# Kernel optimization log

Hardware: AMD Instinct MI355X
Metric: run time of the kernel (lower is better)

## Reference

```python
import jax, jax.numpy as jnp
import numpy as np
from jax import lax

B, T, E, V, U = 128, 80, 100, 10000, 512


def setup_inputs() -> dict:
    key = jax.random.key(0)
    ks = jax.random.split(key, 10)
    s = 0.05
    return {
        "tokens": jax.random.randint(ks[0], (B, T), 0, V, dtype=jnp.int32),
        "emb": jax.random.normal(ks[1], (V, E), jnp.float32) * s,
        "k0": jax.random.normal(ks[2], (E, U), jnp.float32) * s,   # cell0 input kernel
        "rk0": jax.random.normal(ks[3], (U, U), jnp.float32) * s,  # cell0 recurrent kernel
        "b0": jnp.zeros((U,), jnp.float32),
        "k1": jax.random.normal(ks[4], (U, U), jnp.float32) * s,   # cell1 input kernel
        "rk1": jax.random.normal(ks[5], (U, U), jnp.float32) * s,
        "b1": jnp.zeros((U,), jnp.float32),
        "wd": jax.random.normal(ks[6], (U, 1), jnp.float32) * s,   # output Dense
        "bd": jnp.zeros((1,), jnp.float32),
    }


def reference(tokens, emb, k0, rk0, b0, k1, rk1, b1, wd, bd):
    # Embedding lookup: [B, T, E]
    x = emb[tokens]
    xs = jnp.swapaxes(x, 0, 1)  # [T, B, E] for scan over time

    # Source quirk: `state0 = state1` after each step, so from step 1 onward
    # BOTH cells recur on cell1's previous hidden state h. Carry is a single h.
    def step(h, word):
        h0 = jnp.tanh(word @ k0 + h @ rk0 + b0)  # SimpleRNNCell 0 (dropout off: training=None)
        h1 = jnp.tanh(h0 @ k1 + h @ rk1 + b1)    # SimpleRNNCell 1
        return h1, None

    h_init = jnp.zeros((B, U), x.dtype)
    h_last, _ = lax.scan(step, h_init, xs)

    logits = h_last @ wd + bd  # [B, 1]
    return jax.nn.sigmoid(logits)
```

## Files before the change

kernel.cpp:

```cpp
#include <hip/hip_runtime.h>


typedef __attribute__((ext_vector_type(8))) short short8;
typedef __attribute__((ext_vector_type(4))) float f32x4;

#define MFMA16(a,b,c) __builtin_amdgcn_mfma_f32_16x16x32_bf16(a,b,c,0,0,0)
#define LOAD_RLX(p)    __hip_atomic_load((p), __ATOMIC_RELAXED, __HIP_MEMORY_SCOPE_AGENT)
#define STORE_RLX(p,v) __hip_atomic_store((p), (v), __ATOMIC_RELAXED, __HIP_MEMORY_SCOPE_AGENT)
#define ADD_RLX(p,v)   __hip_atomic_fetch_add((p), (v), __ATOMIC_RELAXED, __HIP_MEMORY_SCOPE_AGENT)

__device__ __forceinline__ short f2bf(float v){
  unsigned u = __float_as_uint(v);
  u = (u + 0x7fffu + ((u >> 16) & 1u)) >> 16;
  return (short)u;
}
__device__ __forceinline__ float bf2f(short s){
  return __uint_as_float(((unsigned)(unsigned short)s) << 16);
}
__device__ __forceinline__ float fast_tanh(float x){
  x = fminf(15.f, fmaxf(-15.f, x));
  float e = __expf(2.f * x);
  return (e - 1.f) * __builtin_amdgcn_rcpf(e + 1.f);
}

__launch_bounds__(128, 1)
__global__ void rnn_kernel(const int* __restrict__ tokens,
                           const float* __restrict__ emb,
                           const float* __restrict__ k0,
                           const float* __restrict__ rk0,
                           const float* __restrict__ b0,
                           const float* __restrict__ k1,
                           const float* __restrict__ rk1,
                           const float* __restrict__ b1,
                           const float* __restrict__ wd,
                           const float* __restrict__ bd,
                           float* __restrict__ out,
                           char* __restrict__ ws)
{
  constexpr int T = 80, E = 100, U = 512;
  const int tid  = threadIdx.x;
  const int w    = tid >> 6;
  const int lane = tid & 63;
  const int m    = lane & 15;
  const int q    = lane >> 4;

  __shared__ __align__(16) short sW[6][16][520];
  __shared__ __align__(16) short sH[2][16][520];
  __shared__ __align__(16) short sE[2][16][136];
  __shared__ __align__(16) short sK0[2][16][136];
  __shared__ int   sTok[16][80];
  __shared__ float sB0[16], sB1[16];
  __shared__ float sRed[16][8];
  __shared__ int   sReg[2];

  int*      regCnt = (int*)(ws + 512);
  int*      flags  = (int*)(ws + 4096);
  unsigned* hPk    = (unsigned*)(ws + 40960);
  unsigned* h0Pk   = hPk + 128*U;

  int xcc;
  asm volatile("s_getreg_b32 %0, hwreg(HW_REG_XCC_ID)" : "=s"(xcc));
  if (tid == 0){
    int slot = ADD_RLX(regCnt + (xcc & 7)*16, 1);
    sReg[0] = xcc & 7;
    sReg[1] = slot;
  }
  __syncthreads();
  const int cl  = sReg[0];
  const int mem = sReg[1];
  int* const myFlag   = flags + (cl*32 + mem)*32;
  int* const pollAddr = flags + (cl*32 + (lane & 31))*32;

  const float* mats[3] = { rk0, rk1, k1 };
  for (int mi = 0; mi < 3; ++mi){
    const float* G = mats[mi];
    for (int i = tid; i < 16*U; i += 128){
      int k = i >> 4, c = i & 15;
      float v  = G[k*U + mem*16 + c];
      short hi = f2bf(v);
      short lo = f2bf(v - bf2f(hi));
      sW[2*mi+0][c][k] = hi;
      sW[2*mi+1][c][k] = lo;
    }
  }
  for (int i = tid; i < 2*16*136; i += 128){ ((short*)sE)[i] = 0; ((short*)sK0)[i] = 0; }
  __syncthreads();
  for (int i = tid; i < 16*E; i += 128){
    int e = i >> 4, c = i & 15;
    float v  = k0[e*U + mem*16 + c];
    short hi = f2bf(v);
    short lo = f2bf(v - bf2f(hi));
    sK0[0][c][e] = hi; sK0[1][c][e] = lo;
  }
  for (int i = tid; i < 16*T; i += 128){
    int r = i / T, t = i - r*T;
    sTok[r][t] = tokens[(cl*16 + r)*T + t];
  }
  if (tid < 16){ sB0[tid] = b0[mem*16 + tid]; sB1[tid] = b1[mem*16 + tid]; }
  __syncthreads();

  auto post = [&](int val){
    asm volatile("s_waitcnt vmcnt(0)" ::: "memory");
    if (lane == 0) STORE_RLX(myFlag, val);
  };
  auto pollFlags = [&](int target){
    while (__any(LOAD_RLX(pollAddr) < target)) {}
  };
  auto gather = [&](const unsigned* srcPk){
    const uint4* s = (const uint4*)(srcPk + cl*16*U);
    uint4 r[16];
    #pragma unroll
    for (int j = 0; j < 16; ++j)
      asm volatile("global_load_dwordx4 %0, %1, off sc0"
                   : "=v"(r[j]) : "v"(&s[j*128 + tid]));
    asm volatile("s_waitcnt vmcnt(0)" ::: "memory");
    #pragma unroll
    for (int j = 0; j < 16; ++j){
      int i = j*128 + tid, row = i >> 7, c = (i & 127) * 4;
      unsigned h0 = (r[j].x >> 16)     | (r[j].y & 0xffff0000u);
      unsigned h1 = (r[j].z >> 16)     | (r[j].w & 0xffff0000u);
      unsigned l0 = (r[j].x & 0xffffu) | (r[j].y << 16);
      unsigned l1 = (r[j].z & 0xffffu) | (r[j].w << 16);
      uint2 hh; hh.x = h0; hh.y = h1;
      uint2 ll; ll.x = l0; ll.y = l1;
      *(uint2*)&sH[0][row][c] = hh;
      *(uint2*)&sH[1][row][c] = ll;
    }
  };

  const f32x4 zero4 = {0.f, 0.f, 0.f, 0.f};

  for (int t = 0; t < T; ++t){
    if (w == 1){
      float ev[25];
      #pragma unroll
      for (int p = 0; p < 25; ++p){
        int i = lane + p*64;
        ev[p] = emb[sTok[i/E][t]*E + (i % E)];
      }
      #pragma unroll
      for (int p = 0; p < 25; ++p){
        int i = lane + p*64;
        int row = i / E, e = i % E;
        short hi = f2bf(ev[p]);
        short lo = f2bf(ev[p] - bf2f(hi));
        sE[0][row][e] = hi; sE[1][row][e] = lo;
      }
    } else {
      if (t > 0) pollFlags(2*t);
    }
    __syncthreads();
    if (t > 0) gather(hPk);
    __syncthreads();

    f32x4 z1a = zero4, z1b = zero4, z1c = zero4, z1d = zero4;
    if (w == 0){
      f32x4 za = zero4, zb = zero4, zc = zero4, zd = zero4;
      #pragma unroll
      for (int kk = 0; kk < 4; ++kk){
        short8 ah = *(const short8*)&sE[0][m][kk*32 + q*8];
        short8 al = *(const short8*)&sE[1][m][kk*32 + q*8];
        short8 bh = *(const short8*)&sK0[0][m][kk*32 + q*8];
        short8 bl = *(const short8*)&sK0[1][m][kk*32 + q*8];
        za = MFMA16(ah, bh, za); zb = MFMA16(al, bh, zb);
        zc = MFMA16(ah, bl, zc); zd = MFMA16(al, bl, zd);
      }
      if (t > 0){
        #pragma unroll
        for (int kk = 0; kk < 16; ++kk){
          short8 ah = *(const short8*)&sH[0][m][kk*32 + q*8];
          short8 al = *(const short8*)&sH[1][m][kk*32 + q*8];
          short8 bh = *(const short8*)&sW[0][m][kk*32 + q*8];
          short8 bl = *(const short8*)&sW[1][m][kk*32 + q*8];
          za = MFMA16(ah, bh, za); zb = MFMA16(al, bh, zb);
          zc = MFMA16(ah, bl, zc); zd = MFMA16(al, bl, zd);
        }
      }
      f32x4 z = za; z += zb; z += zc; z += zd;
      #pragma unroll
      for (int r = 0; r < 4; ++r){
        float h0v = fast_tanh(z[r] + sB0[m]);
        short hi = f2bf(h0v);
        short lo = f2bf(h0v - bf2f(hi));
        int gr = cl*16 + q*4 + r, gc = mem*16 + m;
        unsigned pk = ((unsigned)(unsigned short)hi << 16) | (unsigned short)lo;
        h0Pk[gr*U + gc] = pk;
      }
      post(2*t + 1);
    } else {
      if (t > 0){
        #pragma unroll
        for (int kk = 0; kk < 16; ++kk){
          short8 ah = *(const short8*)&sH[0][m][kk*32 + q*8];
          short8 al = *(const short8*)&sH[1][m][kk*32 + q*8];
          short8 bh = *(const short8*)&sW[2][m][kk*32 + q*8];
          short8 bl = *(const short8*)&sW[3][m][kk*32 + q*8];
          z1a = MFMA16(ah, bh, z1a); z1b = MFMA16(al, bh, z1b);
          z1c = MFMA16(ah, bl, z1c); z1d = MFMA16(al, bl, z1d);
        }
      }
    }

    if (w == 0) pollFlags(2*t + 1);
    __syncthreads();
    gather(h0Pk);
    __syncthreads();
    if (w == 1){
      f32x4 za = zero4, zb = zero4, zc = zero4, zd = zero4;
      #pragma unroll
      for (int kk = 0; kk < 16; ++kk){
        short8 ah = *(const short8*)&sH[0][m][kk*32 + q*8];
        short8 al = *(const short8*)&sH[1][m][kk*32 + q*8];
        short8 bh = *(const short8*)&sW[4][m][kk*32 + q*8];
        short8 bl = *(const short8*)&sW[5][m][kk*32 + q*8];
        za = MFMA16(ah, bh, za); zb = MFMA16(al, bh, zb);
        zc = MFMA16(ah, bl, zc); zd = MFMA16(al, bl, zd);
      }
      f32x4 z = za; z += zb; z += zc; z += zd;
      z += z1a; z += z1b; z += z1c; z += z1d;
      #pragma unroll
      for (int r = 0; r < 4; ++r){
        float h1v = fast_tanh(z[r] + sB1[m]);
        short hi = f2bf(h1v);
        short lo = f2bf(h1v - bf2f(hi));
        int gr = cl*16 + q*4 + r, gc = mem*16 + m;
        unsigned pk = ((unsigned)(unsigned short)hi << 16) | (unsigned short)lo;
        hPk[gr*U + gc] = pk;
      }
      post(2*t + 2);
    }
  }

  if (mem == 0){
    if (w == 0) pollFlags(2*T);
    __syncthreads();
    gather(hPk);
    __syncthreads();
    {
      int row = tid >> 3, seg = tid & 7;
      float acc = 0.f;
      for (int u = seg*64; u < seg*64 + 64; ++u){
        float hv = bf2f(sH[0][row][u]) + bf2f(sH[1][row][u]);
        acc += hv * wd[u];
      }
      sRed[row][seg] = acc;
    }
    __syncthreads();
    if (tid < 16){
      float s = bd[0];
      #pragma unroll
      for (int j = 0; j < 8; ++j) s += sRed[tid][j];
      out[cl*16 + tid] = 1.f / (1.f + __expf(-s));
    }
  }

  __threadfence();
}

extern "C" void kernel_launch(void* const* d_in, const int* in_sizes, int n_in,
                              void* d_out, int out_size, void* d_ws, size_t ws_size,
                              hipStream_t stream) {
  const int*   tokens = (const int*)  d_in[0];
  const float* emb    = (const float*)d_in[1];
  const float* k0     = (const float*)d_in[2];
  const float* rk0    = (const float*)d_in[3];
  const float* b0     = (const float*)d_in[4];
  const float* k1     = (const float*)d_in[5];
  const float* rk1    = (const float*)d_in[6];
  const float* b1     = (const float*)d_in[7];
  const float* wd     = (const float*)d_in[8];
  const float* bd     = (const float*)d_in[9];

  hipMemsetAsync(d_ws, 0, 40960, stream);

  hipLaunchKernelGGL(rnn_kernel, dim3(256), dim3(128), 0, stream,
                     tokens, emb, k0, rk0, b0, k1, rk1, b1, wd, bd,
                     (float*)d_out, (char*)d_ws);
}
```

Measured before the change: 625.9 us.

## Split batch rows per wavefront to remove block barriers and use independent flag chains

```diff
diff --git a/kernel.cpp b/kernel.cpp
--- a/kernel.cpp
+++ b/kernel.cpp
@@ -39,18 +39,18 @@
 {
   constexpr int T = 80, E = 100, U = 512;
   const int tid  = threadIdx.x;
-  const int w    = tid >> 6;
+  const int g    = tid >> 6;
   const int lane = tid & 63;
   const int m    = lane & 15;
   const int q    = lane >> 4;
+  const int m7   = m & 7;
 
   __shared__ __align__(16) short sW[6][16][520];
-  __shared__ __align__(16) short sH[2][16][520];
-  __shared__ __align__(16) short sE[2][16][136];
+  __shared__ __align__(16) short sH[2][2][8][520];
+  __shared__ __align__(16) short sE[2][2][8][136];
   __shared__ __align__(16) short sK0[2][16][136];
   __shared__ int   sTok[16][80];
   __shared__ float sB0[16], sB1[16];
-  __shared__ float sRed[16][8];
   __shared__ int   sReg[2];
 
   int*      regCnt = (int*)(ws + 512);
@@ -68,8 +68,8 @@
   __syncthreads();
   const int cl  = sReg[0];
   const int mem = sReg[1];
-  int* const myFlag   = flags + (cl*32 + mem)*32;
-  int* const pollAddr = flags + (cl*32 + (lane & 31))*32;
+  int* const myFlag   = flags + (cl*32 + mem)*32 + g*16;
+  int* const pollAddr = flags + (cl*32 + (lane & 31))*32 + g*16;
 
   const float* mats[3] = { rk0, rk1, k1 };
   for (int mi = 0; mi < 3; ++mi){
@@ -83,7 +83,8 @@
       sW[2*mi+1][c][k] = lo;
     }
   }
-  for (int i = tid; i < 2*16*136; i += 128){ ((short*)sE)[i] = 0; ((short*)sK0)[i] = 0; }
+  for (int i = tid; i < 2*2*8*136; i += 128) ((short*)sE)[i]  = 0;
+  for (int i = tid; i < 2*16*136;  i += 128) ((short*)sK0)[i] = 0;
   __syncthreads();
   for (int i = tid; i < 16*E; i += 128){
     int e = i >> 4, c = i & 15;
@@ -99,6 +100,11 @@
   if (tid < 16){ sB0[tid] = b0[mem*16 + tid]; sB1[tid] = b1[mem*16 + tid]; }
   __syncthreads();
 
+  short (*sHg)[8][520] = sH[g];
+  short (*sEg)[8][136] = sE[g];
+  unsigned* const hRow0  = hPk  + (cl*16 + g*8)*U;
+  unsigned* const h0Row0 = h0Pk + (cl*16 + g*8)*U;
+
   auto post = [&](int val){
     asm volatile("s_waitcnt vmcnt(0)" ::: "memory");
     if (lane == 0) STORE_RLX(myFlag, val);
@@ -106,151 +112,132 @@
   auto pollFlags = [&](int target){
     while (__any(LOAD_RLX(pollAddr) < target)) {}
   };
-  auto gather = [&](const unsigned* srcPk){
-    const uint4* s = (const uint4*)(srcPk + cl*16*U);
+  auto gather = [&](const unsigned* srcRow0){
+    const uint4* s = (const uint4*)srcRow0;
     uint4 r[16];
     #pragma unroll
     for (int j = 0; j < 16; ++j)
       asm volatile("global_load_dwordx4 %0, %1, off sc0"
-                   : "=v"(r[j]) : "v"(&s[j*128 + tid]));
+                   : "=v"(r[j]) : "v"(&s[j*64 + lane]));
     asm volatile("s_waitcnt vmcnt(0)" ::: "memory");
     #pragma unroll
     for (int j = 0; j < 16; ++j){
-      int i = j*128 + tid, row = i >> 7, c = (i & 127) * 4;
+      int i = j*64 + lane, row = i >> 7, c = (i & 127) * 4;
       unsigned h0 = (r[j].x >> 16)     | (r[j].y & 0xffff0000u);
       unsigned h1 = (r[j].z >> 16)     | (r[j].w & 0xffff0000u);
       unsigned l0 = (r[j].x & 0xffffu) | (r[j].y << 16);
       unsigned l1 = (r[j].z & 0xffffu) | (r[j].w << 16);
       uint2 hh; hh.x = h0; hh.y = h1;
       uint2 ll; ll.x = l0; ll.y = l1;
-      *(uint2*)&sH[0][row][c] = hh;
-      *(uint2*)&sH[1][row][c] = ll;
+      *(uint2*)&sHg[0][row][c] = hh;
+      *(uint2*)&sHg[1][row][c] = ll;
     }
   };
 
   const f32x4 zero4 = {0.f, 0.f, 0.f, 0.f};
 
   for (int t = 0; t < T; ++t){
-    if (w == 1){
-      float ev[25];
-      #pragma unroll
-      for (int p = 0; p < 25; ++p){
-        int i = lane + p*64;
-        ev[p] = emb[sTok[i/E][t]*E + (i % E)];
-      }
-      #pragma unroll
-      for (int p = 0; p < 25; ++p){
-        int i = lane + p*64;
-        int row = i / E, e = i % E;
+    float ev[13];
+    #pragma unroll
+    for (int p = 0; p < 13; ++p){
+      int i = lane + p*64;
+      ev[p] = (i < 800) ? emb[sTok[g*8 + i/100][t]*E + (i % 100)] : 0.f;
+    }
+    #pragma unroll
+    for (int p = 0; p < 13; ++p){
+      int i = lane + p*64;
+      if (i < 800){
+        int row = i / 100, e = i % 100;
         short hi = f2bf(ev[p]);
         short lo = f2bf(ev[p] - bf2f(hi));
-        sE[0][row][e] = hi; sE[1][row][e] = lo;
-      }
-    } else {
-      if (t > 0) pollFlags(2*t);
-    }
-    __syncthreads();
-    if (t > 0) gather(hPk);
-    __syncthreads();
-
+        sEg[0][row][e] = hi; sEg[1][row][e] = lo;
+      }
+    }
+    f32x4 za = zero4, zb = zero4, zc = zero4, zd = zero4;
+    #pragma unroll
+    for (int kk = 0; kk < 4; ++kk){
+      short8 ah = *(const short8*)&sEg[0][m7][kk*32 + q*8];
+      short8 al = *(const short8*)&sEg[1][m7][kk*32 + q*8];
+      short8 bh = *(const short8*)&sK0[0][m][kk*32 + q*8];
+      short8 bl = *(const short8*)&sK0[1][m][kk*32 + q*8];
+      za = MFMA16(ah, bh, za); zb = MFMA16(al, bh, zb);
+      zc = MFMA16(ah, bl, zc); zd = MFMA16(al, bl, zd);
+    }
     f32x4 z1a = zero4, z1b = zero4, z1c = zero4, z1d = zero4;
-    if (w == 0){
-      f32x4 za = zero4, zb = zero4, zc = zero4, zd = zero4;
-      #pragma unroll
-      for (int kk = 0; kk < 4; ++kk){
-        short8 ah = *(const short8*)&sE[0][m][kk*32 + q*8];
-        short8 al = *(const short8*)&sE[1][m][kk*32 + q*8];
-        short8 bh = *(const short8*)&sK0[0][m][kk*32 + q*8];
-        short8 bl = *(const short8*)&sK0[1][m][kk*32 + q*8];
-        za = MFMA16(ah, bh, za); zb = MFMA16(al, bh, zb);
-        zc = MFMA16(ah, bl, zc); zd = MFMA16(al, bl, zd);
-      }
-      if (t > 0){
-        #pragma unroll
-        for (int kk = 0; kk < 16; ++kk){
-          short8 ah = *(const short8*)&sH[0][m][kk*32 + q*8];
-          short8 al = *(const short8*)&sH[1][m][kk*32 + q*8];
-          short8 bh = *(const short8*)&sW[0][m][kk*32 + q*8];
-          short8 bl = *(const short8*)&sW[1][m][kk*32 + q*8];
-          za = MFMA16(ah, bh, za); zb = MFMA16(al, bh, zb);
-          zc = MFMA16(ah, bl, zc); zd = MFMA16(al, bl, zd);
-        }
-      }
-      f32x4 z = za; z += zb; z += zc; z += zd;
-      #pragma unroll
-      for (int r = 0; r < 4; ++r){
-        float h0v = fast_tanh(z[r] + sB0[m]);
-        short hi = f2bf(h0v);
-        short lo = f2bf(h0v - bf2f(hi));
-        int gr = cl*16 + q*4 + r, gc = mem*16 + m;
-        unsigned pk = ((unsigned)(unsigned short)hi << 16) | (unsigned short)lo;
-        h0Pk[gr*U + gc] = pk;
-      }
-      post(2*t + 1);
-    } else {
-      if (t > 0){
-        #pragma unroll
-        for (int kk = 0; kk < 16; ++kk){
-          short8 ah = *(const short8*)&sH[0][m][kk*32 + q*8];
-          short8 al = *(const short8*)&sH[1][m][kk*32 + q*8];
-          short8 bh = *(const short8*)&sW[2][m][kk*32 + q*8];
-          short8 bl = *(const short8*)&sW[3][m][kk*32 + q*8];
-          z1a = MFMA16(ah, bh, z1a); z1b = MFMA16(al, bh, z1b);
-          z1c = MFMA16(ah, bl, z1c); z1d = MFMA16(al, bl, z1d);
-        }
-      }
-    }
-
-    if (w == 0) pollFlags(2*t + 1);
-    __syncthreads();
-    gather(h0Pk);
-    __syncthreads();
-    if (w == 1){
-      f32x4 za = zero4, zb = zero4, zc = zero4, zd = zero4;
+    if (t > 0){
+      pollFlags(2*t);
+      gather(hRow0);
       #pragma unroll
       for (int kk = 0; kk < 16; ++kk){
-        short8 ah = *(const short8*)&sH[0][m][kk*32 + q*8];
-        short8 al = *(const short8*)&sH[1][m][kk*32 + q*8];
-        short8 bh = *(const short8*)&sW[4][m][kk*32 + q*8];
-        short8 bl = *(const short8*)&sW[5][m][kk*32 + q*8];
-        za = MFMA16(ah, bh, za); zb = MFMA16(al, bh, zb);
-        zc = MFMA16(ah, bl, zc); zd = MFMA16(al, bl, zd);
-      }
+        short8 ah  = *(const short8*)&sHg[0][m7][kk*32 + q*8];
+        short8 al  = *(const short8*)&sHg[1][m7][kk*32 + q*8];
+        short8 b0h = *(const short8*)&sW[0][m][kk*32 + q*8];
+        short8 b0l = *(const short8*)&sW[1][m][kk*32 + q*8];
+        short8 b1h = *(const short8*)&sW[2][m][kk*32 + q*8];
+        short8 b1l = *(const short8*)&sW[3][m][kk*32 + q*8];
+        za  = MFMA16(ah, b0h, za);  zb  = MFMA16(al, b0h, zb);
+        zc  = MFMA16(ah, b0l, zc);  zd  = MFMA16(al, b0l, zd);
+        z1a = MFMA16(ah, b1h, z1a); z1b = MFMA16(al, b1h, z1b);
+        z1c = MFMA16(ah, b1l, z1c); z1d = MFMA16(al, b1l, z1d);
+      }
+    }
+    {
       f32x4 z = za; z += zb; z += zc; z += zd;
-      z += z1a; z += z1b; z += z1c; z += z1d;
-      #pragma unroll
-      for (int r = 0; r < 4; ++r){
-        float h1v = fast_tanh(z[r] + sB1[m]);
-        short hi = f2bf(h1v);
-        short lo = f2bf(h1v - bf2f(hi));
-        int gr = cl*16 + q*4 + r, gc = mem*16 + m;
-        unsigned pk = ((unsigned)(unsigned short)hi << 16) | (unsigned short)lo;
-        hPk[gr*U + gc] = pk;
+      if (q < 2){
+        #pragma unroll
+        for (int r = 0; r < 4; ++r){
+          float h0v = fast_tanh(z[r] + sB0[m]);
+          short hi = f2bf(h0v);
+          short lo = f2bf(h0v - bf2f(hi));
+          unsigned pk = ((unsigned)(unsigned short)hi << 16) | (unsigned short)lo;
+          h0Row0[(q*4 + r)*U + mem*16 + m] = pk;
+        }
+      }
+      post(2*t + 1);
+    }
+
+    pollFlags(2*t + 1);
+    gather(h0Row0);
+    #pragma unroll
+    for (int kk = 0; kk < 16; ++kk){
+      short8 ah = *(const short8*)&sHg[0][m7][kk*32 + q*8];
+      short8 al = *(const short8*)&sHg[1][m7][kk*32 + q*8];
+      short8 bh = *(const short8*)&sW[4][m][kk*32 + q*8];
+      short8 bl = *(const short8*)&sW[5][m][kk*32 + q*8];
+      z1a = MFMA16(ah, bh, z1a); z1b = MFMA16(al, bh, z1b);
+      z1c = MFMA16(ah, bl, z1c); z1d = MFMA16(al, bl, z1d);
+    }
+    {
+      f32x4 y = z1a; y += z1b; y += z1c; y += z1d;
+      if (q < 2){
+        #pragma unroll
+        for (int r = 0; r < 4; ++r){
+          float h1v = fast_tanh(y[r] + sB1[m]);
+          short hi = f2bf(h1v);
+          short lo = f2bf(h1v - bf2f(hi));
+          unsigned pk = ((unsigned)(unsigned short)hi << 16) | (unsigned short)lo;
+          hRow0[(q*4 + r)*U + mem*16 + m] = pk;
+        }
       }
       post(2*t + 2);
     }
   }
 
   if (mem == 0){
-    if (w == 0) pollFlags(2*T);
-    __syncthreads();
-    gather(hPk);
-    __syncthreads();
-    {
-      int row = tid >> 3, seg = tid & 7;
-      float acc = 0.f;
-      for (int u = seg*64; u < seg*64 + 64; ++u){
-        float hv = bf2f(sH[0][row][u]) + bf2f(sH[1][row][u]);
-        acc += hv * wd[u];
-      }
-      sRed[row][seg] = acc;
-    }
-    __syncthreads();
-    if (tid < 16){
-      float s = bd[0];
-      #pragma unroll
-      for (int j = 0; j < 8; ++j) s += sRed[tid][j];
-      out[cl*16 + tid] = 1.f / (1.f + __expf(-s));
+    pollFlags(2*T);
+    gather(hRow0);
+    int row = lane >> 3, seg = lane & 7;
+    float acc = 0.f;
+    for (int u = seg*64; u < seg*64 + 64; ++u){
+      float hv = bf2f(sHg[0][row][u]) + bf2f(sHg[1][row][u]);
+      acc += hv * wd[u];
+    }
+    acc += __shfl_xor(acc, 1);
+    acc += __shfl_xor(acc, 2);
+    acc += __shfl_xor(acc, 4);
+    if (seg == 0){
+      float s = acc + bd[0];
+      out[cl*16 + g*8 + row] = 1.f / (1.f + __expf(-s));
     }
   }
 
```

New measurement: 686.9 us. 1.1x slower.
